# Performance work log

Measured on AMD Instinct MI355X. Metric: run time of the kernel, lower is better.

The kernel has to match this reference:

```python
import jax, jax.numpy as jnp
import numpy as np

N_NODES = 100000
N_EDGES = 1600000
IN_CH, GCN_CH, OUT_CH = 64, 64, 32


def gcn_conv(x, W, b, row, col, ew):
    """PyG GCNConv: normalize=True, add_self_loops=True (weight 1.0)."""
    N = x.shape[0]
    deg = jax.ops.segment_sum(ew, col, num_segments=N) + 1.0  # self-loop weight 1
    dis = jax.lax.rsqrt(deg)                                   # deg >= 1
    norm = dis[row] * ew * dis[col]                            # [E]
    xw = x @ W                                                 # [N, C_out]
    agg = jax.ops.segment_sum(norm[:, None] * xw[row], col, num_segments=N)
    # self-loop contribution: dis[i] * 1 * dis[i] * xw[i]
    return agg + (dis * dis)[:, None] * xw + b


def setup_inputs() -> dict:
    key = jax.random.key(0)
    ks = jax.random.split(key, 9)
    x = jax.random.normal(ks[0], (N_NODES, IN_CH), dtype=jnp.float32)
    edge_index = jax.random.randint(ks[1], (2, N_EDGES), 0, N_NODES, dtype=jnp.int64)
    edge_weight = jax.random.uniform(ks[2], (N_EDGES,), dtype=jnp.float32)
    s1 = 1.0 / np.sqrt(IN_CH)
    s2 = 1.0 / np.sqrt(GCN_CH)
    W1 = jax.random.uniform(ks[3], (IN_CH, GCN_CH), jnp.float32, -s1, s1)
    b1 = jnp.zeros((GCN_CH,), jnp.float32)
    W2 = jax.random.uniform(ks[4], (GCN_CH, GCN_CH), jnp.float32, -s2, s2)
    b2 = jnp.zeros((GCN_CH,), jnp.float32)
    Wout = jax.random.uniform(ks[5], (GCN_CH, OUT_CH), jnp.float32, -s2, s2)
    bout = jax.random.uniform(ks[6], (OUT_CH,), jnp.float32, -s2, s2)
    return {"x": x, "edge_index": edge_index, "edge_weight": edge_weight,
            "W1": W1, "b1": b1, "W2": W2, "b2": b2, "Wout": Wout, "bout": bout}


def reference(x, edge_index, edge_weight, W1, b1, W2, b2, Wout, bout):
    row, col = edge_index[0], edge_index[1]
    h = jax.nn.relu(gcn_conv(x, W1, b1, row, col, edge_weight))
    h = jax.nn.relu(gcn_conv(h, W2, b2, row, col, edge_weight))
    return jnp.tanh(h @ Wout + bout)
```

## Files before the change

### kernel.cpp

```cpp
#include <hip/hip_runtime.h>
#include <hip/hip_fp16.h>
#include <math.h>

#define N_NODES 100000
#define N_EDGES 1600000
#define IN_CH   64
#define GCN_CH  64
#define OUT_CH  32
#define MAXDEG  48

#define EW_SCALE  32768.0f
#define EW_INV    (1.0f / 32768.0f)

#define BSHIFT   7
#define NBUCK    1024
#define NBUCK_USED ((N_NODES + 127) / 128)
#define EPB      4096
#define NBLK     ((N_EDGES + EPB - 1) / EPB)
#define HIST_TOT (NBUCK * NBLK)
#define NCHUNK   (HIST_TOT / 1024)
#define GEMMB    ((N_NODES + 63) / 64)

typedef _Float16 f16x2 __attribute__((ext_vector_type(2)));

__device__ inline float fdot2(__half2 a, __half2 b, float c) {
    f16x2 av, bv;
    __builtin_memcpy(&av, &a, 4);
    __builtin_memcpy(&bv, &b, 4);
    return __builtin_amdgcn_fdot2(av, bv, c, false);
}

__global__ void hist_kernel(const int* __restrict__ col, unsigned* __restrict__ hist_g) {
    __shared__ unsigned sh[NBUCK];
    int blk = blockIdx.x;
    for (int i = threadIdx.x; i < NBUCK; i += 1024) sh[i] = 0;
    __syncthreads();
    int base = blk * EPB;
    int lim  = min(EPB, N_EDGES - base);
    for (int i = threadIdx.x; i < lim; i += 1024)
        atomicAdd(&sh[(unsigned)col[base + i] >> BSHIFT], 1u);
    __syncthreads();
    for (int b = threadIdx.x; b < NBUCK; b += 1024)
        hist_g[(size_t)b * NBLK + blk] = sh[b];
}

__global__ void scan1_kernel(const unsigned* __restrict__ in, unsigned* __restrict__ outp,
                             unsigned* __restrict__ blockSums) {
    __shared__ unsigned sdata[256];
    int t = threadIdx.x;
    int base = blockIdx.x * 1024 + t * 4;
    unsigned v[4];
    unsigned sum = 0;
#pragma unroll
    for (int i = 0; i < 4; ++i) { v[i] = in[base + i]; sum += v[i]; }
    sdata[t] = sum;
    __syncthreads();
    for (int off = 1; off < 256; off <<= 1) {
        unsigned x = (t >= off) ? sdata[t - off] : 0;
        __syncthreads();
        sdata[t] += x;
        __syncthreads();
    }
    unsigned excl = sdata[t] - sum;
    if (t == 255) blockSums[blockIdx.x] = sdata[t];
    unsigned run = excl;
#pragma unroll
    for (int i = 0; i < 4; ++i) { outp[base + i] = run; run += v[i]; }
}

__device__ inline void chunk_scan(const unsigned* __restrict__ bsum, unsigned* cb,
                                  int t) {
    if (t < 512) cb[t] = (t < NCHUNK) ? bsum[t] : 0u;
    __syncthreads();
    for (int off = 1; off < 512; off <<= 1) {
        unsigned x = 0;
        if (t < 512 && t >= off) x = cb[t - off];
        __syncthreads();
        if (t < 512) cb[t] += x;
        __syncthreads();
    }
}

__global__ void scatter_gemm_kernel(const int* __restrict__ row, const int* __restrict__ col,
                                    const float* __restrict__ ew,
                                    const unsigned* __restrict__ scanned,
                                    const unsigned* __restrict__ blockSums,
                                    unsigned long long* __restrict__ srt,
                                    const float* __restrict__ X, const float* __restrict__ W,
                                    __half* __restrict__ Y) {
    __shared__ unsigned cb[512];
    __shared__ unsigned cur[NBUCK];
    __shared__ unsigned lbase[NBUCK];
    __shared__ unsigned lcur[NBUCK];
    __shared__ unsigned wsum[16];
    __shared__ unsigned long long lrec[EPB];
    __shared__ float4   Ws[64][16];
    int t = threadIdx.x;
    int bid = blockIdx.x;

    if (bid < NBLK) {
        chunk_scan(blockSums, cb, t);
        lcur[t] = 0;
        __syncthreads();

        int blk  = bid;
        int base = blk * EPB;
        int lim  = min(EPB, N_EDGES - base);

        unsigned long long recs[4];
        unsigned bks[4];
#pragma unroll
        for (int k = 0; k < 4; ++k) {
            int i = t + k * 1024;
            bool ok = i < lim;
            int e = base + (ok ? i : 0);
            unsigned c = (unsigned)col[e];
            unsigned r = (unsigned)row[e];
            float    w = ew[e];
            unsigned u15 = min((unsigned)(w * EW_SCALE + 0.5f), 32767u);
            recs[k] = ((unsigned long long)c << 32) | ((r << 15) | u15);
            bks[k]  = c >> BSHIFT;
            if (ok) atomicAdd(&lcur[bks[k]], 1u);
        }
        __syncthreads();

        {
            unsigned v = lcur[t];
            unsigned inc = v;
#pragma unroll
            for (int off = 1; off < 64; off <<= 1) {
                unsigned u = __shfl_up(inc, off, 64);
                if ((t & 63) >= off) inc += u;
            }
            if ((t & 63) == 63) wsum[t >> 6] = inc;
            __syncthreads();
            unsigned wprefix = 0;
            int wid = t >> 6;
            for (int wv = 0; wv < wid; ++wv) wprefix += wsum[wv];
            lbase[t] = wprefix + inc - v;
            size_t hidx = (size_t)t * NBLK + blk;
            unsigned chunk = (unsigned)(hidx >> 10);
            cur[t]  = scanned[hidx] + (chunk ? cb[chunk - 1] : 0u);
            lcur[t] = lbase[t];
        }
        __syncthreads();

#pragma unroll
        for (int k = 0; k < 4; ++k) {
            int i = t + k * 1024;
            if (i < lim) {
                unsigned p = atomicAdd(&lcur[bks[k]], 1u);
                lrec[p] = recs[k];
            }
        }
        __syncthreads();

        for (int j = t; j < lim; j += 1024) {
            unsigned long long v = lrec[j];
            unsigned b = (unsigned)(v >> 32) >> BSHIFT;
            unsigned gpos = cur[b] + ((unsigned)j - lbase[b]);
            srt[gpos] = v;
        }
    } else {
        ((float4*)Ws)[t] = ((const float4*)W)[t];
        __syncthreads();
        int gb  = bid - NBLK;
        int q   = t & 15;
        int sub = t >> 4;
        int rw  = gb * 64 + sub;
        if (rw >= N_NODES) return;
        const float4* xr = (const float4*)(X + (size_t)rw * 64);
        float4 acc = {0.f, 0.f, 0.f, 0.f};
#pragma unroll
        for (int k4 = 0; k4 < 16; ++k4) {
            float4 xv = xr[k4];
#pragma unroll
            for (int j = 0; j < 4; ++j) {
                float xs = (j == 0) ? xv.x : (j == 1) ? xv.y : (j == 2) ? xv.z : xv.w;
                float4 wv = Ws[k4 * 4 + j][q];
                acc.x = fmaf(xs, wv.x, acc.x);
                acc.y = fmaf(xs, wv.y, acc.y);
                acc.z = fmaf(xs, wv.z, acc.z);
                acc.w = fmaf(xs, wv.w, acc.w);
            }
        }
        union { __half2 h[2]; float2 f; } u;
        u.h[0] = __floats2half2_rn(acc.x, acc.y);
        u.h[1] = __floats2half2_rn(acc.z, acc.w);
        *(float2*)(Y + (size_t)rw * 64 + q * 4) = u.f;
    }
}

__global__ void ell_fill_kernel(const unsigned* __restrict__ scanned,
                                const unsigned* __restrict__ blockSums,
                                const unsigned long long* __restrict__ srt,
                                unsigned* __restrict__ ell,
                                unsigned* __restrict__ deg_arr, float* __restrict__ dis) {
    __shared__ unsigned cb[512];
    __shared__ unsigned cur[128];
    __shared__ float    wsum[128];
    int t = threadIdx.x;
    chunk_scan(blockSums, cb, t);
    if (t < 128) { cur[t] = 0; wsum[t] = 0.f; }
    __syncthreads();
    int b = blockIdx.x;
    size_t h0 = (size_t)b * NBLK;
    size_t h1 = (size_t)(b + 1) * NBLK;
    unsigned c0 = (unsigned)(h0 >> 10), c1 = (unsigned)(h1 >> 10);
    unsigned start = scanned[h0] + (c0 ? cb[c0 - 1] : 0u);
    unsigned end   = (b + 1 < NBUCK) ? (scanned[h1] + (c1 ? cb[c1 - 1] : 0u))
                                     : (unsigned)N_EDGES;
    for (unsigned i = start + t; i < end; i += 512) {
        unsigned long long v = srt[i];
        unsigned c   = (unsigned)(v >> 32);
        unsigned rec = (unsigned)v;
        unsigned cl  = c & 127u;
        unsigned k   = atomicAdd(&cur[cl], 1u);
        if (k < MAXDEG) ell[(size_t)c * MAXDEG + k] = rec;
        atomicAdd(&wsum[cl], (float)(rec & 32767u) * EW_INV);
    }
    __syncthreads();
    if (t < 128) {
        int c = b * 128 + t;
        if (c < N_NODES) {
            deg_arr[c] = min(cur[t], (unsigned)MAXDEG);
            dis[c]     = rsqrtf(wsum[t] + 1.0f);
        }
    }
}

__global__ void gemm64h_f16_kernel(const __half* __restrict__ X, const float* __restrict__ W,
                                   __half* __restrict__ Y, int nrows) {
    __shared__ float4 Ws[64][16];
    int t = threadIdx.x;
    for (int i = t; i < 64 * 16; i += 256)
        ((float4*)Ws)[i] = ((const float4*)W)[i];
    __syncthreads();

    int q   = t & 15;
    int sub = t >> 4;
    int row = blockIdx.x * 16 + sub;
    if (row >= nrows) return;
    const float4* xr = (const float4*)(X + (size_t)row * 64);
    float4 acc = {0.f, 0.f, 0.f, 0.f};
#pragma unroll
    for (int k8 = 0; k8 < 8; ++k8) {
        float4 raw = xr[k8];
        const __half2* hp = (const __half2*)&raw;
#pragma unroll
        for (int j = 0; j < 4; ++j) {
            float xs0 = __low2float(hp[j]);
            float xs1 = __high2float(hp[j]);
            float4 w0 = Ws[k8 * 8 + 2 * j][q];
            float4 w1 = Ws[k8 * 8 + 2 * j + 1][q];
            acc.x = fmaf(xs0, w0.x, acc.x); acc.y = fmaf(xs0, w0.y, acc.y);
            acc.z = fmaf(xs0, w0.z, acc.z); acc.w = fmaf(xs0, w0.w, acc.w);
            acc.x = fmaf(xs1, w1.x, acc.x); acc.y = fmaf(xs1, w1.y, acc.y);
            acc.z = fmaf(xs1, w1.z, acc.z); acc.w = fmaf(xs1, w1.w, acc.w);
        }
    }
    union { __half2 h[2]; float2 f; } u;
    u.h[0] = __floats2half2_rn(acc.x, acc.y);
    u.h[1] = __floats2half2_rn(acc.z, acc.w);
    *(float2*)(Y + (size_t)row * 64 + q * 4) = u.f;
}

__device__ inline void make_h_raw(const float* acc, float4 xraw,
                                  const float* b, int q, float dd, float* h) {
    const __half2* hp = (const __half2*)&xraw;
    float4 b0 = *(const float4*)(b + q * 8);
    float4 b1 = *(const float4*)(b + q * 8 + 4);
    float xs[8] = {__low2float(hp[0]), __high2float(hp[0]),
                   __low2float(hp[1]), __high2float(hp[1]),
                   __low2float(hp[2]), __high2float(hp[2]),
                   __low2float(hp[3]), __high2float(hp[3])};
    float bb[8] = {b0.x, b0.y, b0.z, b0.w, b1.x, b1.y, b1.z, b1.w};
#pragma unroll
    for (int i = 0; i < 8; ++i)
        h[i] = fmaxf(fmaf(dd, xs[i], acc[i]) + bb[i], 0.f);
}

__device__ inline void fma_pk(float4 raw, __half2 nv, __half2* acc) {
    const __half2* ha = (const __half2*)&raw;
    acc[0] = __hfma2(nv, ha[0], acc[0]);
    acc[1] = __hfma2(nv, ha[1], acc[1]);
    acc[2] = __hfma2(nv, ha[2], acc[2]);
    acc[3] = __hfma2(nv, ha[3], acc[3]);
}

__device__ inline void gather_core(int node, int lane,
                                   const unsigned* __restrict__ deg_arr,
                                   const unsigned* __restrict__ ell,
                                   const __half* __restrict__ XWh,
                                   const float* __restrict__ dis,
                                   float& dc_out, float4& xself, float* accf) {
    int half = lane >> 5;
    int l    = lane & 31;
    int g    = l >> 3;
    int q    = l & 7;
    int base = half << 5;

    int deg = (int)deg_arr[node];
    const unsigned* erow = ell + (size_t)node * MAXDEG;
    unsigned rec1 = (l < deg) ? erow[l] : 0u;
    unsigned rec2 = (l < 16 && 32 + l < deg) ? erow[32 + l] : 0u;
    float dc = dis[node];
    dc_out = dc;

    int   src1 = (int)(rec1 >> 15);
    float nv1  = dis[src1] * ((float)(rec1 & 32767u) * EW_INV) * dc;
    int   src2 = (int)(rec2 >> 15);
    float nv2  = dis[src2] * ((float)(rec2 & 32767u) * EW_INV) * dc;
    __half2 t1 = __float2half2_rn(nv1), t2 = __float2half2_rn(nv2);
    int nv1pk, nv2pk;
    __builtin_memcpy(&nv1pk, &t1, 4);
    __builtin_memcpy(&nv2pk, &t2, 4);

    xself = *(const float4*)(XWh + (size_t)node * 64 + q * 8);

    int dmax = max(deg, __shfl_xor(deg, 32, 64));

    __half2 acc[4] = {__float2half2_rn(0.f), __float2half2_rn(0.f),
                      __float2half2_rn(0.f), __float2half2_rn(0.f)};
    int s1 = min(dmax, 32);
    for (int s = 0; s < s1; s += 16) {
        int srcA  = __shfl(src1,  base + s + g, 64);
        int nvA_i = __shfl(nv1pk, base + s + g, 64);
        int srcB  = __shfl(src1,  base + s + 4 + g, 64);
        int nvB_i = __shfl(nv1pk, base + s + 4 + g, 64);
        int srcC  = __shfl(src1,  base + s + 8 + g, 64);
        int nvC_i = __shfl(nv1pk, base + s + 8 + g, 64);
        int srcD  = __shfl(src1,  base + s + 12 + g, 64);
        int nvD_i = __shfl(nv1pk, base + s + 12 + g, 64);
        float4 rawA = *(const float4*)(XWh + (size_t)srcA * 64 + q * 8);
        float4 rawB = *(const float4*)(XWh + (size_t)srcB * 64 + q * 8);
        float4 rawC = *(const float4*)(XWh + (size_t)srcC * 64 + q * 8);
        float4 rawD = *(const float4*)(XWh + (size_t)srcD * 64 + q * 8);
        __half2 nvA, nvB, nvC, nvD;
        __builtin_memcpy(&nvA, &nvA_i, 4);
        __builtin_memcpy(&nvB, &nvB_i, 4);
        __builtin_memcpy(&nvC, &nvC_i, 4);
        __builtin_memcpy(&nvD, &nvD_i, 4);
        fma_pk(rawA, nvA, acc);
        fma_pk(rawB, nvB, acc);
        fma_pk(rawC, nvC, acc);
        fma_pk(rawD, nvD, acc);
    }
    if (dmax > 32) {
        for (int s = 32; s < dmax; s += 4) {
            int srcB  = __shfl(src2,  base + (s - 32) + g, 64);
            int nvB_i = __shfl(nv2pk, base + (s - 32) + g, 64);
            float4 raw = *(const float4*)(XWh + (size_t)srcB * 64 + q * 8);
            __half2 nvB; __builtin_memcpy(&nvB, &nvB_i, 4);
            fma_pk(raw, nvB, acc);
        }
    }
#pragma unroll
    for (int m = 8; m <= 16; m <<= 1) {
#pragma unroll
        for (int i = 0; i < 4; ++i) {
            int ai; __builtin_memcpy(&ai, &acc[i], 4);
            int bi = __shfl_xor(ai, m, 64);
            __half2 bh; __builtin_memcpy(&bh, &bi, 4);
            acc[i] = __hadd2(acc[i], bh);
        }
    }
#pragma unroll
    for (int i = 0; i < 4; ++i) {
        accf[2 * i]     = __low2float(acc[i]);
        accf[2 * i + 1] = __high2float(acc[i]);
    }
}

__global__ void gather_h_kernel(const unsigned* __restrict__ deg_arr,
                                const unsigned* __restrict__ ell,
                                const __half* __restrict__ XWh,
                                const float* __restrict__ dis, const float* __restrict__ b,
                                __half* __restrict__ H) {
    int lane = threadIdx.x & 63;
    int node = blockIdx.x * 16 + (threadIdx.x >> 6) * 2 + (lane >> 5);
    int l = lane & 31;
    int q = l & 7;

    float dc; float4 xself; float accf[8];
    gather_core(node, lane, deg_arr, ell, XWh, dis, dc, xself, accf);

    if ((l >> 3) == 0) {
        float h[8];
        make_h_raw(accf, xself, b, q, dc * dc, h);
        union { __half2 hh[4]; float4 f; } u;
        u.hh[0] = __floats2half2_rn(h[0], h[1]);
        u.hh[1] = __floats2half2_rn(h[2], h[3]);
        u.hh[2] = __floats2half2_rn(h[4], h[5]);
        u.hh[3] = __floats2half2_rn(h[6], h[7]);
        *(float4*)(H + (size_t)node * 64 + q * 8) = u.f;
    }
}

__global__ void gather_out_kernel(const unsigned* __restrict__ deg_arr,
                                  const unsigned* __restrict__ ell,
                                  const __half* __restrict__ XWh,
                                  const float* __restrict__ dis, const float* __restrict__ b,
                                  const float* __restrict__ Wout, const float* __restrict__ bout,
                                  float* __restrict__ OUT) {
    __shared__ __half2 Ws2[32][32];
    {
        for (int idx = threadIdx.x; idx < 32 * 32; idx += (int)blockDim.x) {
            int kp = idx >> 5, j = idx & 31;
            Ws2[kp][j] = __floats2half2_rn(Wout[(2 * kp) * OUT_CH + j],
                                           Wout[(2 * kp + 1) * OUT_CH + j]);
        }
        __syncthreads();
    }

    int lane = threadIdx.x & 63;
    int node = blockIdx.x * 16 + (threadIdx.x >> 6) * 2 + (lane >> 5);
    int half = lane >> 5;
    int l = lane & 31;
    int q = l & 7;
    int base = half << 5;

    float dc; float4 xself; float accf[8];
    gather_core(node, lane, deg_arr, ell, XWh, dis, dc, xself, accf);

    float h[8];
    make_h_raw(accf, xself, b, q, dc * dc, h);

    int hpk[4];
#pragma unroll
    for (int i = 0; i < 4; ++i) {
        __half2 t2 = __floats2half2_rn(h[2 * i], h[2 * i + 1]);
        __builtin_memcpy(&hpk[i], &t2, 4);
    }
    float partial = 0.f;
#pragma unroll
    for (int kk = 0; kk < 32; ++kk) {
        int hv_i = __shfl(hpk[kk & 3], base + (kk >> 2), 64);
        __half2 hv; __builtin_memcpy(&hv, &hv_i, 4);
        partial = fdot2(hv, Ws2[kk][l], partial);
    }
    float v = partial + bout[l];
    float e = __expf(2.f * v);
    OUT[(size_t)node * OUT_CH + l] = 1.f - 2.f / (e + 1.f);
}

extern "C" void kernel_launch(void* const* d_in, const int* in_sizes, int n_in,
                              void* d_out, int out_size, void* d_ws, size_t ws_size,
                              hipStream_t stream) {
    const float* x     = (const float*)d_in[0];
    const int*   eidx  = (const int*)  d_in[1];
    const float* ew    = (const float*)d_in[2];
    const float* W1    = (const float*)d_in[3];
    const float* b1    = (const float*)d_in[4];
    const float* W2    = (const float*)d_in[5];
    const float* b2    = (const float*)d_in[6];
    const float* Wout  = (const float*)d_in[7];
    const float* bout  = (const float*)d_in[8];
    float*       out   = (float*)d_out;

    const int* row = eidx;
    const int* col = eidx + N_EDGES;

    char*  ws   = (char*)d_ws;
    size_t offs = 0;
    auto alloc = [&](size_t bytes) {
        char* p = ws + offs;
        offs += (bytes + 1023) & ~(size_t)1023;
        return p;
    };
    unsigned* hist_g    = (unsigned*)alloc((size_t)HIST_TOT * sizeof(unsigned));
    unsigned* scanned   = (unsigned*)alloc((size_t)HIST_TOT * sizeof(unsigned));
    unsigned* blockSums = (unsigned*)alloc((size_t)NCHUNK * sizeof(unsigned));
    unsigned long long* srt = (unsigned long long*)alloc((size_t)N_EDGES * 8);
    unsigned* deg_arr   = (unsigned*)alloc((size_t)N_NODES * sizeof(unsigned));
    float*    dis       = (float*)   alloc((size_t)N_NODES * sizeof(float));
    unsigned* ell       = (unsigned*)alloc((size_t)N_NODES * MAXDEG * sizeof(unsigned));
    __half*   xwh       = (__half*)  alloc((size_t)N_NODES * GCN_CH * sizeof(__half));
    __half*   hbuf      = (__half*)srt;

    const int BLK  = 256;
    const int BLKG = 512;
    const int gGemm   = (N_NODES + 15) / 16;
    const int gGather = N_NODES / 16;

    hist_kernel<<<NBLK, 1024, 0, stream>>>(col, hist_g);
    scan1_kernel<<<NCHUNK, 256, 0, stream>>>(hist_g, scanned, blockSums);
    scatter_gemm_kernel<<<NBLK + GEMMB, 1024, 0, stream>>>(row, col, ew, scanned,
                                                           blockSums, srt, x, W1, xwh);
    ell_fill_kernel<<<NBUCK_USED, 512, 0, stream>>>(scanned, blockSums, srt,
                                                    ell, deg_arr, dis);

    gather_h_kernel<<<gGather, BLKG, 0, stream>>>(deg_arr, ell, xwh, dis, b1, hbuf);

    gemm64h_f16_kernel<<<gGemm, BLK, 0, stream>>>(hbuf, W2, xwh, N_NODES);
    gather_out_kernel<<<gGather, BLKG, 0, stream>>>(deg_arr, ell, xwh, dis, b2,
                                                    Wout, bout, out);
}
```

Baseline: 152.8 us.

## Split XW table into channel chunks and gather per chunk for cache locality

The XW feature table is stored channel-chunked (8 chunks of 8 halves per node), and the gather kernels are replaced by one chunked gather kernel where each block handles a single chunk, so the working set per pass is 1.6MB and can stay in cache. The fused output GEMM inside the second gather is moved into a separate out_gemm kernel that reads the stored hidden activations. In exchange, ELL records and dis lookups are re-read 8 times (once per chunk), there is an extra kernel launch, and an extra H2 round trip through memory.

```diff
diff --git a/kernel.cpp b/kernel.cpp
--- a/kernel.cpp
+++ b/kernel.cpp
@@ -21,14 +21,10 @@
 #define NCHUNK   (HIST_TOT / 1024)
 #define GEMMB    ((N_NODES + 63) / 64)
 
-typedef _Float16 f16x2 __attribute__((ext_vector_type(2)));
-
-__device__ inline float fdot2(__half2 a, __half2 b, float c) {
-    f16x2 av, bv;
-    __builtin_memcpy(&av, &a, 4);
-    __builtin_memcpy(&bv, &b, 4);
-    return __builtin_amdgcn_fdot2(av, bv, c, false);
-}
+#define NCH        8
+#define NPB        32
+#define GGATHER    (N_NODES / NPB * NCH)
+#define GOUT       (N_NODES / 32)
 
 __global__ void hist_kernel(const int* __restrict__ col, unsigned* __restrict__ hist_g) {
     __shared__ unsigned sh[NBUCK];
@@ -187,7 +183,9 @@
         union { __half2 h[2]; float2 f; } u;
         u.h[0] = __floats2half2_rn(acc.x, acc.y);
         u.h[1] = __floats2half2_rn(acc.z, acc.w);
-        *(float2*)(Y + (size_t)rw * 64 + q * 4) = u.f;
+        int ch  = q >> 1;
+        int off = (q & 1) * 4;
+        *(float2*)(Y + ((size_t)ch * N_NODES + rw) * 8 + off) = u.f;
     }
 }
 
@@ -262,22 +260,9 @@
     union { __half2 h[2]; float2 f; } u;
     u.h[0] = __floats2half2_rn(acc.x, acc.y);
     u.h[1] = __floats2half2_rn(acc.z, acc.w);
-    *(float2*)(Y + (size_t)row * 64 + q * 4) = u.f;
-}
-
-__device__ inline void make_h_raw(const float* acc, float4 xraw,
-                                  const float* b, int q, float dd, float* h) {
-    const __half2* hp = (const __half2*)&xraw;
-    float4 b0 = *(const float4*)(b + q * 8);
-    float4 b1 = *(const float4*)(b + q * 8 + 4);
-    float xs[8] = {__low2float(hp[0]), __high2float(hp[0]),
-                   __low2float(hp[1]), __high2float(hp[1]),
-                   __low2float(hp[2]), __high2float(hp[2]),
-                   __low2float(hp[3]), __high2float(hp[3])};
-    float bb[8] = {b0.x, b0.y, b0.z, b0.w, b1.x, b1.y, b1.z, b1.w};
-#pragma unroll
-    for (int i = 0; i < 8; ++i)
-        h[i] = fmaxf(fmaf(dd, xs[i], acc[i]) + bb[i], 0.f);
+    int ch  = q >> 1;
+    int off = (q & 1) * 4;
+    *(float2*)(Y + ((size_t)ch * N_NODES + row) * 8 + off) = u.f;
 }
 
 __device__ inline void fma_pk(float4 raw, __half2 nv, __half2* acc) {
@@ -288,75 +273,36 @@
     acc[3] = __hfma2(nv, ha[3], acc[3]);
 }
 
-__device__ inline void gather_core(int node, int lane,
-                                   const unsigned* __restrict__ deg_arr,
-                                   const unsigned* __restrict__ ell,
-                                   const __half* __restrict__ XWh,
-                                   const float* __restrict__ dis,
-                                   float& dc_out, float4& xself, float* accf) {
-    int half = lane >> 5;
-    int l    = lane & 31;
-    int g    = l >> 3;
-    int q    = l & 7;
-    int base = half << 5;
-
-    int deg = (int)deg_arr[node];
-    const unsigned* erow = ell + (size_t)node * MAXDEG;
-    unsigned rec1 = (l < deg) ? erow[l] : 0u;
-    unsigned rec2 = (l < 16 && 32 + l < deg) ? erow[32 + l] : 0u;
-    float dc = dis[node];
-    dc_out = dc;
-
-    int   src1 = (int)(rec1 >> 15);
-    float nv1  = dis[src1] * ((float)(rec1 & 32767u) * EW_INV) * dc;
-    int   src2 = (int)(rec2 >> 15);
-    float nv2  = dis[src2] * ((float)(rec2 & 32767u) * EW_INV) * dc;
-    __half2 t1 = __float2half2_rn(nv1), t2 = __float2half2_rn(nv2);
-    int nv1pk, nv2pk;
-    __builtin_memcpy(&nv1pk, &t1, 4);
-    __builtin_memcpy(&nv2pk, &t2, 4);
-
-    xself = *(const float4*)(XWh + (size_t)node * 64 + q * 8);
-
-    int dmax = max(deg, __shfl_xor(deg, 32, 64));
+__global__ void gather_chunk_kernel(const unsigned* __restrict__ deg_arr,
+                                    const unsigned* __restrict__ ell,
+                                    const __half* __restrict__ tbl,
+                                    const float* __restrict__ dis,
+                                    const float* __restrict__ b,
+                                    __half* __restrict__ H) {
+    int bid   = blockIdx.x;
+    int chunk = bid & 7;
+    int grp   = bid >> 3;
+    int t     = threadIdx.x;
+    int lane  = t & 63;
+    int le    = lane & 15;
+    int node  = grp * NPB + (t >> 6) * 4 + (lane >> 4);
+    int deg   = (int)deg_arr[node];
+    float dc  = dis[node];
+    const unsigned* erow  = ell + (size_t)node * MAXDEG;
+    const __half*   tbase = tbl + (size_t)chunk * N_NODES * 8;
 
     __half2 acc[4] = {__float2half2_rn(0.f), __float2half2_rn(0.f),
                       __float2half2_rn(0.f), __float2half2_rn(0.f)};
-    int s1 = min(dmax, 32);
-    for (int s = 0; s < s1; s += 16) {
-        int srcA  = __shfl(src1,  base + s + g, 64);
-        int nvA_i = __shfl(nv1pk, base + s + g, 64);
-        int srcB  = __shfl(src1,  base + s + 4 + g, 64);
-        int nvB_i = __shfl(nv1pk, base + s + 4 + g, 64);
-        int srcC  = __shfl(src1,  base + s + 8 + g, 64);
-        int nvC_i = __shfl(nv1pk, base + s + 8 + g, 64);
-        int srcD  = __shfl(src1,  base + s + 12 + g, 64);
-        int nvD_i = __shfl(nv1pk, base + s + 12 + g, 64);
-        float4 rawA = *(const float4*)(XWh + (size_t)srcA * 64 + q * 8);
-        float4 rawB = *(const float4*)(XWh + (size_t)srcB * 64 + q * 8);
-        float4 rawC = *(const float4*)(XWh + (size_t)srcC * 64 + q * 8);
-        float4 rawD = *(const float4*)(XWh + (size_t)srcD * 64 + q * 8);
-        __half2 nvA, nvB, nvC, nvD;
-        __builtin_memcpy(&nvA, &nvA_i, 4);
-        __builtin_memcpy(&nvB, &nvB_i, 4);
-        __builtin_memcpy(&nvC, &nvC_i, 4);
-        __builtin_memcpy(&nvD, &nvD_i, 4);
-        fma_pk(rawA, nvA, acc);
-        fma_pk(rawB, nvB, acc);
-        fma_pk(rawC, nvC, acc);
-        fma_pk(rawD, nvD, acc);
-    }
-    if (dmax > 32) {
-        for (int s = 32; s < dmax; s += 4) {
-            int srcB  = __shfl(src2,  base + (s - 32) + g, 64);
-            int nvB_i = __shfl(nv2pk, base + (s - 32) + g, 64);
-            float4 raw = *(const float4*)(XWh + (size_t)srcB * 64 + q * 8);
-            __half2 nvB; __builtin_memcpy(&nvB, &nvB_i, 4);
-            fma_pk(raw, nvB, acc);
-        }
-    }
-#pragma unroll
-    for (int m = 8; m <= 16; m <<= 1) {
+    for (int s = le; s < deg; s += 16) {
+        unsigned rec = erow[s];
+        int   src = (int)(rec >> 15);
+        float nv  = dis[src] * ((float)(rec & 32767u) * EW_INV) * dc;
+        __half2 nvh = __float2half2_rn(nv);
+        float4 raw = *(const float4*)(tbase + (size_t)src * 8);
+        fma_pk(raw, nvh, acc);
+    }
+#pragma unroll
+    for (int m = 1; m <= 8; m <<= 1) {
 #pragma unroll
         for (int i = 0; i < 4; ++i) {
             int ai; __builtin_memcpy(&ai, &acc[i], 4);
@@ -365,83 +311,66 @@
             acc[i] = __hadd2(acc[i], bh);
         }
     }
-#pragma unroll
-    for (int i = 0; i < 4; ++i) {
-        accf[2 * i]     = __low2float(acc[i]);
-        accf[2 * i + 1] = __high2float(acc[i]);
-    }
-}
-
-__global__ void gather_h_kernel(const unsigned* __restrict__ deg_arr,
-                                const unsigned* __restrict__ ell,
-                                const __half* __restrict__ XWh,
-                                const float* __restrict__ dis, const float* __restrict__ b,
-                                __half* __restrict__ H) {
-    int lane = threadIdx.x & 63;
-    int node = blockIdx.x * 16 + (threadIdx.x >> 6) * 2 + (lane >> 5);
-    int l = lane & 31;
-    int q = l & 7;
-
-    float dc; float4 xself; float accf[8];
-    gather_core(node, lane, deg_arr, ell, XWh, dis, dc, xself, accf);
-
-    if ((l >> 3) == 0) {
+    if (le == 0) {
+        float dd = dc * dc;
+        float4 xraw = *(const float4*)(tbase + (size_t)node * 8);
+        const __half2* hp = (const __half2*)&xraw;
+        float4 b0 = *(const float4*)(b + chunk * 8);
+        float4 b1 = *(const float4*)(b + chunk * 8 + 4);
+        float bb[8] = {b0.x, b0.y, b0.z, b0.w, b1.x, b1.y, b1.z, b1.w};
         float h[8];
-        make_h_raw(accf, xself, b, q, dc * dc, h);
+#pragma unroll
+        for (int i = 0; i < 4; ++i) {
+            float a0 = __low2float(acc[i]),  a1 = __high2float(acc[i]);
+            float x0 = __low2float(hp[i]),   x1 = __high2float(hp[i]);
+            h[2 * i]     = fmaxf(fmaf(dd, x0, a0) + bb[2 * i], 0.f);
+            h[2 * i + 1] = fmaxf(fmaf(dd, x1, a1) + bb[2 * i + 1], 0.f);
+        }
         union { __half2 hh[4]; float4 f; } u;
         u.hh[0] = __floats2half2_rn(h[0], h[1]);
         u.hh[1] = __floats2half2_rn(h[2], h[3]);
         u.hh[2] = __floats2half2_rn(h[4], h[5]);
         u.hh[3] = __floats2half2_rn(h[6], h[7]);
-        *(float4*)(H + (size_t)node * 64 + q * 8) = u.f;
-    }
-}
-
-__global__ void gather_out_kernel(const unsigned* __restrict__ deg_arr,
-                                  const unsigned* __restrict__ ell,
-                                  const __half* __restrict__ XWh,
-                                  const float* __restrict__ dis, const float* __restrict__ b,
-                                  const float* __restrict__ Wout, const float* __restrict__ bout,
-                                  float* __restrict__ OUT) {
-    __shared__ __half2 Ws2[32][32];
-    {
-        for (int idx = threadIdx.x; idx < 32 * 32; idx += (int)blockDim.x) {
-            int kp = idx >> 5, j = idx & 31;
-            Ws2[kp][j] = __floats2half2_rn(Wout[(2 * kp) * OUT_CH + j],
-                                           Wout[(2 * kp + 1) * OUT_CH + j]);
-        }
-        __syncthreads();
-    }
-
-    int lane = threadIdx.x & 63;
-    int node = blockIdx.x * 16 + (threadIdx.x >> 6) * 2 + (lane >> 5);
-    int half = lane >> 5;
-    int l = lane & 31;
-    int q = l & 7;
-    int base = half << 5;
-
-    float dc; float4 xself; float accf[8];
-    gather_core(node, lane, deg_arr, ell, XWh, dis, dc, xself, accf);
-
-    float h[8];
-    make_h_raw(accf, xself, b, q, dc * dc, h);
-
-    int hpk[4];
-#pragma unroll
-    for (int i = 0; i < 4; ++i) {
-        __half2 t2 = __floats2half2_rn(h[2 * i], h[2 * i + 1]);
-        __builtin_memcpy(&hpk[i], &t2, 4);
-    }
-    float partial = 0.f;
-#pragma unroll
-    for (int kk = 0; kk < 32; ++kk) {
-        int hv_i = __shfl(hpk[kk & 3], base + (kk >> 2), 64);
-        __half2 hv; __builtin_memcpy(&hv, &hv_i, 4);
-        partial = fdot2(hv, Ws2[kk][l], partial);
-    }
-    float v = partial + bout[l];
-    float e = __expf(2.f * v);
-    OUT[(size_t)node * OUT_CH + l] = 1.f - 2.f / (e + 1.f);
+        *(float4*)(H + (size_t)node * 64 + chunk * 8) = u.f;
+    }
+}
+
+__global__ void out_gemm_kernel(const __half* __restrict__ H2, const float* __restrict__ Wout,
+                                const float* __restrict__ bout, float* __restrict__ OUT) {
+    __shared__ float4 Ws4[64][8];
+    int t = threadIdx.x;
+    for (int i = t; i < 512; i += 256)
+        ((float4*)Ws4)[i] = ((const float4*)Wout)[i];
+    __syncthreads();
+
+    int q   = t & 7;
+    int sub = t >> 3;
+    int rw  = blockIdx.x * 32 + sub;
+    if (rw >= N_NODES) return;
+    const float4* hr = (const float4*)(H2 + (size_t)rw * 64);
+    float4 acc = *(const float4*)(bout + q * 4);
+#pragma unroll
+    for (int k8 = 0; k8 < 8; ++k8) {
+        float4 raw = hr[k8];
+        const __half2* hp = (const __half2*)&raw;
+#pragma unroll
+        for (int j = 0; j < 4; ++j) {
+            float xs0 = __low2float(hp[j]);
+            float xs1 = __high2float(hp[j]);
+            float4 w0 = Ws4[k8 * 8 + 2 * j][q];
+            float4 w1 = Ws4[k8 * 8 + 2 * j + 1][q];
+            acc.x = fmaf(xs0, w0.x, acc.x); acc.y = fmaf(xs0, w0.y, acc.y);
+            acc.z = fmaf(xs0, w0.z, acc.z); acc.w = fmaf(xs0, w0.w, acc.w);
+            acc.x = fmaf(xs1, w1.x, acc.x); acc.y = fmaf(xs1, w1.y, acc.y);
+            acc.z = fmaf(xs1, w1.z, acc.z); acc.w = fmaf(xs1, w1.w, acc.w);
+        }
+    }
+    float4 v;
+    v.x = 1.f - 2.f / (__expf(2.f * acc.x) + 1.f);
+    v.y = 1.f - 2.f / (__expf(2.f * acc.y) + 1.f);
+    v.z = 1.f - 2.f / (__expf(2.f * acc.z) + 1.f);
+    v.w = 1.f - 2.f / (__expf(2.f * acc.w) + 1.f);
+    *(float4*)(OUT + (size_t)rw * OUT_CH + q * 4) = v;
 }
 
 extern "C" void kernel_launch(void* const* d_in, const int* in_sizes, int n_in,
@@ -475,24 +404,23 @@
     unsigned* deg_arr   = (unsigned*)alloc((size_t)N_NODES * sizeof(unsigned));
     float*    dis       = (float*)   alloc((size_t)N_NODES * sizeof(float));
     unsigned* ell       = (unsigned*)alloc((size_t)N_NODES * MAXDEG * sizeof(unsigned));
-    __half*   xwh       = (__half*)  alloc((size_t)N_NODES * GCN_CH * sizeof(__half));
+    __half*   xwc       = (__half*)  alloc((size_t)NCH * N_NODES * 8 * sizeof(__half));
     __half*   hbuf      = (__half*)srt;
 
     const int BLK  = 256;
-    const int BLKG = 512;
-    const int gGemm   = (N_NODES + 15) / 16;
-    const int gGather = N_NODES / 16;
+    const int gGemm = (N_NODES + 15) / 16;
 
     hist_kernel<<<NBLK, 1024, 0, stream>>>(col, hist_g);
     scan1_kernel<<<NCHUNK, 256, 0, stream>>>(hist_g, scanned, blockSums);
     scatter_gemm_kernel<<<NBLK + GEMMB, 1024, 0, stream>>>(row, col, ew, scanned,
-                                                           blockSums, srt, x, W1, xwh);
+                                                           blockSums, srt, x, W1, xwc);
     ell_fill_kernel<<<NBUCK_USED, 512, 0, stream>>>(scanned, blockSums, srt,
                                                     ell, deg_arr, dis);
 
-    gather_h_kernel<<<gGather, BLKG, 0, stream>>>(deg_arr, ell, xwh, dis, b1, hbuf);
-
-    gemm64h_f16_kernel<<<gGemm, BLK, 0, stream>>>(hbuf, W2, xwh, N_NODES);
-    gather_out_kernel<<<gGather, BLKG, 0, stream>>>(deg_arr, ell, xwh, dis, b2,
-                                                    Wout, bout, out);
-}
+    gather_chunk_kernel<<<GGATHER, 512, 0, stream>>>(deg_arr, ell, xwc, dis, b1, hbuf);
+
+    gemm64h_f16_kernel<<<gGemm, BLK, 0, stream>>>(hbuf, W2, xwc, N_NODES);
+    gather_chunk_kernel<<<GGATHER, 512, 0, stream>>>(deg_arr, ell, xwc, dis, b2, hbuf);
+
+    out_gemm_kernel<<<GOUT, BLK, 0, stream>>>(hbuf, Wout, bout, out);
+}
```

After: 324.2 us. 112% more time.
